# Performance work log

Hardware: AMD Instinct MI355X
Metric: run time of the kernel (lower is better)

The kernel has to match this reference:

```python
import jax, jax.numpy as jnp
import numpy as np

L, H, D, DK, FF = 3, 8, 128, 16, 512  # layers, heads, embed, key/val dim, ffn hidden
B, N, F_IN, OUT = 32, 512, 16, 3
SCALE = 1.0 / np.sqrt(DK)


def setup_inputs() -> dict:
    key = jax.random.key(0)
    ks = jax.random.split(key, 16)
    x = jax.random.normal(ks[0], (B, N, F_IN), dtype=jnp.float32)
    m = jax.random.randint(ks[1], (B, N, N), 0, 2).astype(jnp.int32)
    # guarantee each query attends to at least itself (avoid all -inf rows)
    m = jnp.maximum(m, jnp.eye(N, dtype=jnp.int32)[None])
    def u(k, shape, fan):
        s = 1.0 / np.sqrt(fan)
        return jax.random.uniform(k, shape, jnp.float32, -s, s)
    return {
        "x": x, "mask": m,
        "We": u(ks[2], (F_IN, D), D),
        "Wq": u(ks[3], (L, H, D, DK), DK),
        "Wk": u(ks[4], (L, H, D, DK), DK),
        "Wv": u(ks[5], (L, H, D, DK), DK),
        "Wout": u(ks[6], (L, H, DK, D), D),
        "Wff1": u(ks[7], (L, D, FF), D),
        "bff1": u(ks[8], (L, FF), D),
        "Wff2": u(ks[9], (L, FF, D), FF),
        "bff2": u(ks[10], (L, D), FF),
        "Wp": u(ks[11], (D, D), D),
        "Wr": u(ks[12], (2 * D, OUT), 2 * D),
        "br": u(ks[13], (OUT,), 2 * D),
    }


def reference(x, mask, We, Wq, Wk, Wv, Wout, Wff1, bff1, Wff2, bff2, Wp, Wr, br):
    mb = mask.astype(bool)[None]  # [1,B,N,N] broadcast over heads
    h = jax.nn.relu(x @ We)  # initial embedding [B,N,D]
    for l in range(L):
        # multi-head attention with additive skip
        Q = jnp.einsum('bnd,hdk->hbnk', h, Wq[l])
        K = jnp.einsum('bnd,hdk->hbnk', h, Wk[l])
        V = jnp.einsum('bnd,hdk->hbnk', h, Wv[l])
        compat = SCALE * jnp.einsum('hbqk,hbnk->hbqn', Q, K)  # [H,B,N,N]
        compat = jnp.where(mb, compat, -jnp.inf)
        attn = jax.nn.softmax(compat, axis=-1)
        # note: torch's attn.clone()[...] = 0 is a no-op, so no re-zeroing
        heads = jnp.einsum('hbqn,hbnk->hbqk', attn, V)
        h = h + jnp.einsum('hbqk,hkd->bqd', heads, Wout[l])
        # feed-forward with additive skip
        h = h + jax.nn.relu(h @ Wff1[l] + bff1[l]) @ Wff2[l] + bff2[l] * 0 + (jax.nn.relu(h @ Wff1[l] + bff1[l]) @ Wff2[l] + bff2[l] - (jax.nn.relu(h @ Wff1[l] + bff1[l]) @ Wff2[l]))  # placeholder removed below
    return h


# clean faithful version (used)
def reference(x, mask, We, Wq, Wk, Wv, Wout, Wff1, bff1, Wff2, bff2, Wp, Wr, br):
    mb = mask.astype(bool)[None]  # [1,B,N,N]
    h = jax.nn.relu(x @ We)  # [B,N,D]
    for l in range(L):
        Q = jnp.einsum('bnd,hdk->hbnk', h, Wq[l])
        K = jnp.einsum('bnd,hdk->hbnk', h, Wk[l])
        V = jnp.einsum('bnd,hdk->hbnk', h, Wv[l])
        compat = SCALE * jnp.einsum('hbqk,hbnk->hbqn', Q, K)
        compat = jnp.where(mb, compat, -jnp.inf)
        attn = jax.nn.softmax(compat, axis=-1)
        heads = jnp.einsum('hbqn,hbnk->hbqk', attn, V)
        h = h + jnp.einsum('hbqk,hkd->bqd', heads, Wout[l])
        h = h + (jax.nn.relu(h @ Wff1[l] + bff1[l]) @ Wff2[l] + bff2[l])
    # readout (actor head: output_dim=3)
    h_pooled = (h.mean(axis=1)) @ Wp  # [B,D]
    f_pooled = jnp.broadcast_to(h_pooled[:, None, :], h.shape)  # [B,N,D]
    features = jax.nn.relu(jnp.concatenate([f_pooled, h], axis=-1))  # [B,N,2D]
    return features @ Wr + br  # [B,N,3]
```

## Files before the change

### kernel.cpp

```cpp
#include <hip/hip_runtime.h>
#include <cstdint>
#include <cstddef>

#define L_LAYERS 3
#define H_HEADS 8
#define D_EMB 128
#define DKV 16
#define FF_DIM 512
#define B_BATCH 32
#define N_SEQ 512
#define F_INP 16
#define OUT_DIM 3
#define M_ROWS (B_BATCH * N_SEQ)
#define QSCALE 0.3606737602222409f

typedef unsigned short ushort_t;
typedef unsigned int uint_t;
typedef __attribute__((ext_vector_type(8))) short short8;
typedef __attribute__((ext_vector_type(4))) float f32x4;
typedef __attribute__((ext_vector_type(16))) float f32x16;

__device__ inline ushort_t f2bf(float x) {
    union { float f; uint_t u; } v; v.f = x;
    uint_t r = v.u + 0x7fffu + ((v.u >> 16) & 1u);
    return (ushort_t)(r >> 16);
}

__device__ inline uint_t pack2bf_tr(float a, float b) {
    union { float f; uint_t u; } ua, ub;
    ua.f = a; ub.f = b;
    return (ua.u >> 16) | (ub.u & 0xffff0000u);
}

__device__ inline float exp2fast(float x) {
#if __has_builtin(__builtin_amdgcn_exp2f)
    return __builtin_amdgcn_exp2f(x);
#else
    float r; __asm__("v_exp_f32 %0, %1" : "=v"(r) : "v"(x)); return r;
#endif
}

__device__ inline void gload16(const void* g, void* l) {
    __builtin_amdgcn_global_load_lds(
        (const __attribute__((address_space(1))) unsigned int*)g,
        (__attribute__((address_space(3))) unsigned int*)l, 16, 0, 0);
}

#define PM_BLK 32768
#define RQ_BLK 576
#define TW_BLK 192
#define T1_BLK 768
#define T2_BLK 768
#define PB_BLK 16
#define EM_BLK 8192
__global__ __launch_bounds__(256) void preproc_kernel(
        const int* __restrict__ mask, unsigned long long* __restrict__ pm,
        const float* __restrict__ Wq, const float* __restrict__ Wk,
        const float* __restrict__ Wv, ushort_t* __restrict__ wqkvT,
        const float* __restrict__ Wout, ushort_t* __restrict__ woutT,
        const float* __restrict__ Wff1, ushort_t* __restrict__ wff1T,
        const float* __restrict__ Wff2, ushort_t* __restrict__ wff2T,
        float* __restrict__ pbsum,
        const float* __restrict__ x, const float* __restrict__ We,
        float* __restrict__ hf, ushort_t* __restrict__ hb) {
    int bx = blockIdx.x;
    const int tid = threadIdx.x;
    if (bx < PM_BLK) {
        int gid = bx * 256 + tid;
        int v = mask[gid];
        unsigned long long bal = __ballot(v != 0);
        if ((tid & 63) == 0) pm[gid >> 6] = bal;
        return;
    }
    bx -= PM_BLK;
    if (bx < RQ_BLK) {
        int idx = bx * 256 + tid;
        int d = idx & 127;
        int n = (idx >> 7) % 384;
        int l = idx / (384 * 128);
        int proj = n >> 7, hh = (n & 127) >> 4, kk = n & 15;
        const float* src = proj == 0 ? Wq : proj == 1 ? Wk : Wv;
        wqkvT[idx] = f2bf(src[((size_t)(l * 8 + hh) * 128 + d) * 16 + kk]);
        return;
    }
    bx -= RQ_BLK;
    if (bx < TW_BLK + T1_BLK + T2_BLK) {
        const float* src; ushort_t* dst; int R, C;
        if (bx < TW_BLK) { src = Wout; dst = woutT; R = 128; C = 128; }
        else if (bx < TW_BLK + T1_BLK) { src = Wff1; dst = wff1T; R = 128; C = 512; bx -= TW_BLK; }
        else { src = Wff2; dst = wff2T; R = 512; C = 128; bx -= TW_BLK + T1_BLK; }
        int idx = bx * 256 + tid;
        int b = idx / (R * C);
        int rem = idx - b * (R * C);
        int r = rem / C, c = rem - r * C;
        dst[(size_t)b * R * C + (size_t)c * R + r] = f2bf(src[idx]);
        return;
    }
    bx -= TW_BLK + T1_BLK + T2_BLK;
    if (bx < PB_BLK) {
        pbsum[bx * 256 + tid] = 0.f;
        return;
    }
    bx -= PB_BLK;
    {
        const int d = tid & 127;
        const int m = bx * 2 + (tid >> 7);
        const float* xr = x + (size_t)m * 16;
        float acc = 0.f;
#pragma unroll
        for (int k = 0; k < 16; k++) acc += xr[k] * We[k * 128 + d];
        acc = fmaxf(acc, 0.f);
        hf[(size_t)m * 128 + d] = acc;
        hb[(size_t)m * 128 + d] = f2bf(acc);
    }
}

__global__ __launch_bounds__(512, 2) void qkv_attn_kernel(
        const ushort_t* __restrict__ hb,
        const ushort_t* __restrict__ WqkvT,
        const uint_t* __restrict__ pm,
        ushort_t* __restrict__ Aout) {
    __shared__ __align__(16) ushort_t sm[26752];
    ushort_t* KF = sm;
    ushort_t* Vt = sm + 8192;
    ushort_t* Qs = sm + 16512;
    ushort_t* Ws = sm + 20608;
    ushort_t* Ps = sm + 16512;

    const int tid = threadIdx.x;
    const int w = tid >> 6, L = tid & 63;
    const int lr = L & 15, lq = L >> 4;
    const int lane31 = L & 31, lhalf = L >> 5;
    const int bx = blockIdx.x;
    const int b = bx >> 4, h = (bx >> 1) & 7, half = bx & 1;

    for (int i = tid; i < 768; i += 512) {
        const int row = i >> 4, cg = i & 15;
        const int proj = row >> 4, kk = row & 15;
        gload16(WqkvT + (size_t)(proj * 128 + h * 16 + kk) * 128 + cg * 8, &Ws[i * 8]);
    }
    __syncthreads();

    const ushort_t* Ab = hb + (size_t)b * 512 * 128;
    for (int mc = 0; mc < 4; mc++) {
        f32x4 acc[3];
#pragma unroll
        for (int j = 0; j < 3; j++) acc[j] = (f32x4){0.f, 0.f, 0.f, 0.f};
#pragma unroll
        for (int k0 = 0; k0 < 128; k0 += 32) {
            short8 af = *(const short8*)(Ab + (size_t)(mc * 128 + w * 16 + lr) * 128 + k0 + lq * 8);
#pragma unroll
            for (int j = 0; j < 3; j++) {
                short8 bf = *(const short8*)&Ws[(j * 16 + lr) * 128 + k0 + lq * 8];
                acc[j] = __builtin_amdgcn_mfma_f32_16x16x32_bf16(af, bf, acc[j], 0, 0, 0);
            }
        }
        const int rbase = mc * 128 + w * 16 + lq * 4;
#pragma unroll
        for (int r = 0; r < 4; r++) {
            const int key = rbase + r;
            KF[(key >> 5) * 512 + ((lr >> 3) * 32 + (key & 31)) * 8 + (lr & 7)] = f2bf(acc[1][r]);
            Vt[lr * 520 + key] = f2bf(acc[2][r]);
        }
        if ((mc >> 1) == half) {
            const int qb = (mc & 1) * 128 + w * 16 + lq * 4;
#pragma unroll
            for (int r = 0; r < 4; r++)
                Qs[(qb + r) * 16 + lr] = f2bf(acc[0][r] * QSCALE);
        }
    }
    __syncthreads();

    const int q0g = half * 256 + w * 32;
    const short8 qf = *(const short8*)&Qs[(w * 32 + lane31) * 16 + lhalf * 8];
    const uint_t* pmr = pm + (size_t)(b * 512 + q0g + lane31) * 16;
    const uint4 mwa = *(const uint4*)(pmr);
    const uint4 mwb = *(const uint4*)(pmr + 4);
    const uint4 mwc = *(const uint4*)(pmr + 8);
    const uint4 mwd = *(const uint4*)(pmr + 12);
    const uint_t mw[16] = {mwa.x, mwa.y, mwa.z, mwa.w, mwb.x, mwb.y, mwb.z, mwb.w,
                           mwc.x, mwc.y, mwc.z, mwc.w, mwd.x, mwd.y, mwd.z, mwd.w};
    __syncthreads();

    const f32x16 zero16 = (f32x16)(0.f);
    short8 vone;
#pragma unroll
    for (int i = 0; i < 8; i++) vone[i] = (short)0x3F80;

    f32x4 oacc0 = (f32x4){0.f, 0.f, 0.f, 0.f};
    f32x4 oacc1 = (f32x4){0.f, 0.f, 0.f, 0.f};
    f32x4 lacc0 = (f32x4){0.f, 0.f, 0.f, 0.f};
    f32x4 lacc1 = (f32x4){0.f, 0.f, 0.f, 0.f};
#pragma unroll
    for (int t = 0; t < 16; t++) {
        short8 kf = *(const short8*)&KF[t * 512 + L * 8];
        f32x16 s = __builtin_amdgcn_mfma_f32_32x32x16_bf16(kf, qf, zero16, 0, 0, 0);
        const uint_t word = mw[t];
#pragma unroll
        for (int r = 0; r < 16; r++) {
            const int keyl = (r & 3) + 8 * (r >> 2) + 4 * lhalf;
            const float e = exp2fast(s[r]);
            s[r] = (word & (1u << keyl)) ? e : 0.f;
        }
#pragma unroll
        for (int g = 0; g < 4; g++) {
            const uint_t lo = pack2bf_tr(s[g * 4 + 0], s[g * 4 + 1]);
            const uint_t hi = pack2bf_tr(s[g * 4 + 2], s[g * 4 + 3]);
            *(uint2*)&Ps[w * 1152 + lane31 * 36 + g * 8 + 4 * lhalf] = make_uint2(lo, hi);
        }
        short8 vb = *(const short8*)&Vt[lr * 520 + t * 32 + lq * 8];
        short8 pa0 = *(const short8*)&Ps[w * 1152 + lr * 36 + lq * 8];
        short8 pa1 = *(const short8*)&Ps[w * 1152 + (16 + lr) * 36 + lq * 8];
        oacc0 = __builtin_amdgcn_mfma_f32_16x16x32_bf16(pa0, vb, oacc0, 0, 0, 0);
        oacc1 = __builtin_amdgcn_mfma_f32_16x16x32_bf16(pa1, vb, oacc1, 0, 0, 0);
        lacc0 = __builtin_amdgcn_mfma_f32_16x16x32_bf16(pa0, vone, lacc0, 0, 0, 0);
        lacc1 = __builtin_amdgcn_mfma_f32_16x16x32_bf16(pa1, vone, lacc1, 0, 0, 0);
    }

#pragma unroll
    for (int qa = 0; qa < 2; qa++) {
        const f32x4 oa = qa ? oacc1 : oacc0;
        const f32x4 la = qa ? lacc1 : lacc0;
#pragma unroll
        for (int rr = 0; rr < 4; rr++) {
            const int qloc = qa * 16 + lq * 4 + rr;
            Aout[(size_t)(b * 512 + q0g + qloc) * 128 + h * 16 + lr] = f2bf(oa[rr] / la[rr]);
        }
    }
}

__global__ __launch_bounds__(256, 2) void tail_kernel(
        const ushort_t* __restrict__ A,
        const ushort_t* __restrict__ WoT,
        const ushort_t* __restrict__ W1T,
        const ushort_t* __restrict__ W2T,
        const float* __restrict__ b1,
        const float* __restrict__ b2,
        float* __restrict__ hf, ushort_t* __restrict__ hb,
        float* __restrict__ pbsum, int accum) {
    __shared__ __align__(16) ushort_t sm[38400];
    ushort_t* As  = sm;
    ushort_t* Bs  = sm + 1024;
    ushort_t* C1b = sm + 17408;
    ushort_t* T   = sm + 21760;

    const int tid = threadIdx.x;
    const int w = tid >> 6, l = tid & 63;
    const int lr = l & 15, lq = l >> 4;
    const int srow = (l >> 2);
    const int scol = (l & 3) * 8;
    const int m0 = blockIdx.x * 32;

    f32x4 c1a[2][2];
#pragma unroll
    for (int i = 0; i < 2; i++)
#pragma unroll
        for (int j = 0; j < 2; j++) c1a[i][j] = (f32x4){0.f, 0.f, 0.f, 0.f};
    for (int k0 = 0; k0 < 128; k0 += 32) {
        if (w < 2)
            gload16(A + (size_t)(m0 + w * 16 + srow) * 128 + k0 + scol,
                    &As[(w * 16 + srow) * 32 + scol]);
#pragma unroll
        for (int it = 0; it < 2; it++)
            gload16(WoT + (size_t)(it * 64 + w * 16 + srow) * 128 + k0 + scol,
                    &Bs[(it * 64 + w * 16 + srow) * 32 + scol]);
        __syncthreads();
        short8 af[2], bfr[2];
#pragma unroll
        for (int i = 0; i < 2; i++) af[i] = *(const short8*)&As[(i * 16 + lr) * 32 + lq * 8];
#pragma unroll
        for (int j = 0; j < 2; j++) bfr[j] = *(const short8*)&Bs[(w * 32 + j * 16 + lr) * 32 + lq * 8];
#pragma unroll
        for (int i = 0; i < 2; i++)
#pragma unroll
            for (int j = 0; j < 2; j++)
                c1a[i][j] = __builtin_amdgcn_mfma_f32_16x16x32_bf16(af[i], bfr[j], c1a[i][j], 0, 0, 0);
        __syncthreads();
    }
    float c1[2][2][4];
#pragma unroll
    for (int i = 0; i < 2; i++)
#pragma unroll
        for (int r = 0; r < 4; r++) {
            const int row = i * 16 + lq * 4 + r;
#pragma unroll
            for (int j = 0; j < 2; j++) {
                const int n = w * 32 + j * 16 + lr;
                const float v = c1a[i][j][r] + hf[(size_t)(m0 + row) * 128 + n];
                c1[i][j][r] = v;
                C1b[row * 136 + n] = f2bf(v);
            }
        }
    __syncthreads();

    f32x4 ta[2][8];
#pragma unroll
    for (int i = 0; i < 2; i++)
#pragma unroll
        for (int j = 0; j < 8; j++) ta[i][j] = (f32x4){0.f, 0.f, 0.f, 0.f};
    for (int k0 = 0; k0 < 128; k0 += 32) {
#pragma unroll
        for (int it = 0; it < 8; it++)
            gload16(W1T + (size_t)(it * 64 + w * 16 + srow) * 128 + k0 + scol,
                    &Bs[(it * 64 + w * 16 + srow) * 32 + scol]);
        __syncthreads();
        short8 af[2], bfr[8];
#pragma unroll
        for (int i = 0; i < 2; i++) af[i] = *(const short8*)&C1b[(i * 16 + lr) * 136 + k0 + lq * 8];
#pragma unroll
        for (int j = 0; j < 8; j++) bfr[j] = *(const short8*)&Bs[(w * 128 + j * 16 + lr) * 32 + lq * 8];
#pragma unroll
        for (int i = 0; i < 2; i++)
#pragma unroll
            for (int j = 0; j < 8; j++)
                ta[i][j] = __builtin_amdgcn_mfma_f32_16x16x32_bf16(af[i], bfr[j], ta[i][j], 0, 0, 0);
        __syncthreads();
    }
#pragma unroll
    for (int j = 0; j < 8; j++) {
        const int n = w * 128 + j * 16 + lr;
        const float bv = b1[n];
#pragma unroll
        for (int i = 0; i < 2; i++)
#pragma unroll
            for (int r = 0; r < 4; r++) {
                const int row = i * 16 + lq * 4 + r;
                T[row * 520 + n] = f2bf(fmaxf(ta[i][j][r] + bv, 0.f));
            }
    }
    __syncthreads();

    f32x4 oa[2][2];
#pragma unroll
    for (int i = 0; i < 2; i++)
#pragma unroll
        for (int j = 0; j < 2; j++) oa[i][j] = (f32x4){0.f, 0.f, 0.f, 0.f};
    for (int k0 = 0; k0 < 512; k0 += 32) {
#pragma unroll
        for (int it = 0; it < 2; it++)
            gload16(W2T + (size_t)(it * 64 + w * 16 + srow) * 512 + k0 + scol,
                    &Bs[(it * 64 + w * 16 + srow) * 32 + scol]);
        __syncthreads();
        short8 af[2], bfr[2];
#pragma unroll
        for (int i = 0; i < 2; i++) af[i] = *(const short8*)&T[(i * 16 + lr) * 520 + k0 + lq * 8];
#pragma unroll
        for (int j = 0; j < 2; j++) bfr[j] = *(const short8*)&Bs[(w * 32 + j * 16 + lr) * 32 + lq * 8];
#pragma unroll
        for (int i = 0; i < 2; i++)
#pragma unroll
            for (int j = 0; j < 2; j++)
                oa[i][j] = __builtin_amdgcn_mfma_f32_16x16x32_bf16(af[i], bfr[j], oa[i][j], 0, 0, 0);
        __syncthreads();
    }
#pragma unroll
    for (int j = 0; j < 2; j++) {
        const int n = w * 32 + j * 16 + lr;
        const float bv = b2[n];
        float psum = 0.f;
#pragma unroll
        for (int i = 0; i < 2; i++)
#pragma unroll
            for (int r = 0; r < 4; r++) {
                const int row = i * 16 + lq * 4 + r;
                const float v = oa[i][j][r] + bv + c1[i][j][r];
                psum += v;
                hf[(size_t)(m0 + row) * 128 + n] = v;
                hb[(size_t)(m0 + row) * 128 + n] = f2bf(v);
            }
        if (accum) {
            psum += __shfl_xor(psum, 16);
            psum += __shfl_xor(psum, 32);
            if (lq == 0) atomicAdd(&pbsum[(m0 >> 9) * 128 + n], psum);
        }
    }
}

__global__ __launch_bounds__(256) void readout_kernel(const float* __restrict__ h,
                                                      const float* __restrict__ pbsum,
                                                      const float* __restrict__ Wp,
                                                      const float* __restrict__ Wr,
                                                      const float* __restrict__ br,
                                                      float* __restrict__ out) {
    const int u = blockIdx.x;
    const int b = u >> 4;
    const int m0 = u * 32;
    const int t = threadIdx.x;
    __shared__ float pooled[128];
    __shared__ float rp[128];
    __shared__ float pb3[3];
    if (t < 128) pooled[t] = pbsum[b * 128 + t] * (1.0f / 512.0f);
    __syncthreads();
    if (t < 128) {
        float a = 0.f;
        for (int dd = 0; dd < 128; dd++) a += pooled[dd] * Wp[dd * 128 + t];
        rp[t] = fmaxf(a, 0.f);
    }
    __syncthreads();
    if (t < OUT_DIM) {
        float a = br[t];
        for (int j = 0; j < 128; j++) a += rp[j] * Wr[j * 3 + t];
        pb3[t] = a;
    }
    __syncthreads();
    const int j = t & 7;
    const int row = m0 + (t >> 3);
    const float* hr = h + (size_t)row * 128 + j * 16;
    float a0 = 0.f, a1 = 0.f, a2o = 0.f;
#pragma unroll
    for (int dd = 0; dd < 16; dd++) {
        const float v = fmaxf(hr[dd], 0.f);
        const float* wr = Wr + (size_t)(128 + j * 16 + dd) * 3;
        a0 += v * wr[0]; a1 += v * wr[1]; a2o += v * wr[2];
    }
#pragma unroll
    for (int off = 4; off; off >>= 1) {
        a0 += __shfl_down(a0, off, 8);
        a1 += __shfl_down(a1, off, 8);
        a2o += __shfl_down(a2o, off, 8);
    }
    if (j == 0) {
        out[(size_t)row * 3 + 0] = a0 + pb3[0];
        out[(size_t)row * 3 + 1] = a1 + pb3[1];
        out[(size_t)row * 3 + 2] = a2o + pb3[2];
    }
}

extern "C" void kernel_launch(void* const* d_in, const int* in_sizes, int n_in,
                              void* d_out, int out_size, void* d_ws, size_t ws_size,
                              hipStream_t stream) {
    const float* x    = (const float*)d_in[0];
    const int*   mask = (const int*)d_in[1];
    const float* We   = (const float*)d_in[2];
    const float* Wq   = (const float*)d_in[3];
    const float* Wk   = (const float*)d_in[4];
    const float* Wv   = (const float*)d_in[5];
    const float* Wout = (const float*)d_in[6];
    const float* Wff1 = (const float*)d_in[7];
    const float* bff1 = (const float*)d_in[8];
    const float* Wff2 = (const float*)d_in[9];
    const float* bff2 = (const float*)d_in[10];
    const float* Wp   = (const float*)d_in[11];
    const float* Wr   = (const float*)d_in[12];
    const float* br   = (const float*)d_in[13];
    float* out = (float*)d_out;

    char* ws = (char*)d_ws;
    unsigned long long* pm64 = (unsigned long long*)(ws + 0);
    const uint_t* pm32       = (const uint_t*)(ws + 0);
    ushort_t* wqkvT = (ushort_t*)(ws + 1048576);
    ushort_t* woutT = (ushort_t*)(ws + 1343488);
    ushort_t* wff1T = (ushort_t*)(ws + 1441792);
    ushort_t* wff2T = (ushort_t*)(ws + 1835008);
    float*    pbsum = (float*)(ws + 2228224);
    float*    hbuf  = (float*)(ws + 4194304);
    ushort_t* hb16  = (ushort_t*)(ws + 12582912);
    ushort_t* a16   = (ushort_t*)(ws + 41943040);

    preproc_kernel<<<PM_BLK + RQ_BLK + TW_BLK + T1_BLK + T2_BLK + PB_BLK + EM_BLK, 256, 0, stream>>>(
        mask, pm64, Wq, Wk, Wv, wqkvT, Wout, woutT, Wff1, wff1T, Wff2, wff2T,
        pbsum, x, We, hbuf, hb16);

    for (int l = 0; l < L_LAYERS; l++) {
        qkv_attn_kernel<<<512, 512, 0, stream>>>(
            hb16, wqkvT + (size_t)l * 384 * 128, pm32, a16);
        tail_kernel<<<M_ROWS / 32, 256, 0, stream>>>(
            a16, woutT + (size_t)l * 128 * 128, wff1T + (size_t)l * 512 * 128,
            wff2T + (size_t)l * 128 * 512, bff1 + l * 512, bff2 + l * 128,
            hbuf, hb16, pbsum, (l == L_LAYERS - 1) ? 1 : 0);
    }

    readout_kernel<<<512, 256, 0, stream>>>(hbuf, pbsum, Wp, Wr, br, out);
}
```

Before: 277.0 us.

## Double-buffer weight tiles in tail kernel and split FF1 into two column halves

Converts the three GEMM stages in tail_kernel to double-buffered shared-memory staging. Each iteration prefetches the next K-slice of A/WoT, W1T or W2T into the alternate buffer, which overlaps global loads with MFMA work and leaves one barrier per iteration instead of two. To fit two W1T buffers, the FF1 stage is split into two 256-column halves with half as many accumulators. Shared memory grows slightly, and the prefetch issued right before the C1b and T writes relies on the next loop's barrier for ordering.

```diff
diff --git a/kernel.cpp b/kernel.cpp
--- a/kernel.cpp
+++ b/kernel.cpp
@@ -238,11 +238,13 @@
         const float* __restrict__ b2,
         float* __restrict__ hf, ushort_t* __restrict__ hb,
         float* __restrict__ pbsum, int accum) {
-    __shared__ __align__(16) ushort_t sm[38400];
-    ushort_t* As  = sm;
-    ushort_t* Bs  = sm + 1024;
-    ushort_t* C1b = sm + 17408;
-    ushort_t* T   = sm + 21760;
+    __shared__ __align__(16) ushort_t sm[39424];
+    ushort_t* AsA = sm;
+    ushort_t* AsB = sm + 1024;
+    ushort_t* BsA = sm + 2048;
+    ushort_t* BsB = sm + 10240;
+    ushort_t* C1b = sm + 18432;
+    ushort_t* T   = sm + 22784;
 
     const int tid = threadIdx.x;
     const int w = tid >> 6, l = tid & 63;
@@ -256,26 +258,37 @@
     for (int i = 0; i < 2; i++)
 #pragma unroll
         for (int j = 0; j < 2; j++) c1a[i][j] = (f32x4){0.f, 0.f, 0.f, 0.f};
+    if (w < 2)
+        gload16(A + (size_t)(m0 + w * 16 + srow) * 128 + scol, &AsA[(w * 16 + srow) * 32 + scol]);
+#pragma unroll
+    for (int it = 0; it < 2; it++)
+        gload16(WoT + (size_t)(it * 64 + w * 16 + srow) * 128 + scol, &BsA[(it * 64 + w * 16 + srow) * 32 + scol]);
+#pragma unroll
     for (int k0 = 0; k0 < 128; k0 += 32) {
-        if (w < 2)
-            gload16(A + (size_t)(m0 + w * 16 + srow) * 128 + k0 + scol,
-                    &As[(w * 16 + srow) * 32 + scol]);
-#pragma unroll
-        for (int it = 0; it < 2; it++)
-            gload16(WoT + (size_t)(it * 64 + w * 16 + srow) * 128 + k0 + scol,
-                    &Bs[(it * 64 + w * 16 + srow) * 32 + scol]);
+        ushort_t* Ac = (k0 & 32) ? AsB : AsA;
+        ushort_t* Bc = (k0 & 32) ? BsB : BsA;
+        ushort_t* An = (k0 & 32) ? AsA : AsB;
+        ushort_t* Bn = (k0 & 32) ? BsA : BsB;
         __syncthreads();
+        if (k0 + 32 < 128) {
+            if (w < 2)
+                gload16(A + (size_t)(m0 + w * 16 + srow) * 128 + k0 + 32 + scol,
+                        &An[(w * 16 + srow) * 32 + scol]);
+#pragma unroll
+            for (int it = 0; it < 2; it++)
+                gload16(WoT + (size_t)(it * 64 + w * 16 + srow) * 128 + k0 + 32 + scol,
+                        &Bn[(it * 64 + w * 16 + srow) * 32 + scol]);
+        }
         short8 af[2], bfr[2];
 #pragma unroll
-        for (int i = 0; i < 2; i++) af[i] = *(const short8*)&As[(i * 16 + lr) * 32 + lq * 8];
-#pragma unroll
-        for (int j = 0; j < 2; j++) bfr[j] = *(const short8*)&Bs[(w * 32 + j * 16 + lr) * 32 + lq * 8];
+        for (int i = 0; i < 2; i++) af[i] = *(const short8*)&Ac[(i * 16 + lr) * 32 + lq * 8];
+#pragma unroll
+        for (int j = 0; j < 2; j++) bfr[j] = *(const short8*)&Bc[(w * 32 + j * 16 + lr) * 32 + lq * 8];
 #pragma unroll
         for (int i = 0; i < 2; i++)
 #pragma unroll
             for (int j = 0; j < 2; j++)
                 c1a[i][j] = __builtin_amdgcn_mfma_f32_16x16x32_bf16(af[i], bfr[j], c1a[i][j], 0, 0, 0);
-        __syncthreads();
     }
     float c1[2][2][4];
 #pragma unroll
@@ -291,67 +304,88 @@
                 C1b[row * 136 + n] = f2bf(v);
             }
         }
-    __syncthreads();
-
-    f32x4 ta[2][8];
+
+#pragma unroll
+    for (int it = 0; it < 4; it++)
+        gload16(W1T + (size_t)(it * 64 + w * 16 + srow) * 128 + scol, &BsA[(it * 64 + w * 16 + srow) * 32 + scol]);
+#pragma unroll
+    for (int nc = 0; nc < 2; nc++) {
+        f32x4 ta[2][4];
+#pragma unroll
+        for (int i = 0; i < 2; i++)
+#pragma unroll
+            for (int j = 0; j < 4; j++) ta[i][j] = (f32x4){0.f, 0.f, 0.f, 0.f};
+#pragma unroll
+        for (int k0i = 0; k0i < 4; k0i++) {
+            const int c = nc * 4 + k0i;
+            ushort_t* Bc = (c & 1) ? BsB : BsA;
+            ushort_t* Bn = (c & 1) ? BsA : BsB;
+            __syncthreads();
+            if (c + 1 < 8) {
+                const int nc2 = (c + 1) >> 2, k02 = ((c + 1) & 3) * 32;
+#pragma unroll
+                for (int it = 0; it < 4; it++)
+                    gload16(W1T + (size_t)(nc2 * 256 + it * 64 + w * 16 + srow) * 128 + k02 + scol,
+                            &Bn[(it * 64 + w * 16 + srow) * 32 + scol]);
+            }
+            short8 af[2], bfr[4];
+#pragma unroll
+            for (int i = 0; i < 2; i++)
+                af[i] = *(const short8*)&C1b[(i * 16 + lr) * 136 + k0i * 32 + lq * 8];
+#pragma unroll
+            for (int j = 0; j < 4; j++)
+                bfr[j] = *(const short8*)&Bc[(w * 64 + j * 16 + lr) * 32 + lq * 8];
+#pragma unroll
+            for (int i = 0; i < 2; i++)
+#pragma unroll
+                for (int j = 0; j < 4; j++)
+                    ta[i][j] = __builtin_amdgcn_mfma_f32_16x16x32_bf16(af[i], bfr[j], ta[i][j], 0, 0, 0);
+        }
+#pragma unroll
+        for (int j = 0; j < 4; j++) {
+            const int n = nc * 256 + w * 64 + j * 16 + lr;
+            const float bv = b1[n];
+#pragma unroll
+            for (int i = 0; i < 2; i++)
+#pragma unroll
+                for (int r = 0; r < 4; r++) {
+                    const int row = i * 16 + lq * 4 + r;
+                    T[row * 520 + n] = f2bf(fmaxf(ta[i][j][r] + bv, 0.f));
+                }
+        }
+    }
+
+#pragma unroll
+    for (int it = 0; it < 2; it++)
+        gload16(W2T + (size_t)(it * 64 + w * 16 + srow) * 512 + scol, &BsA[(it * 64 + w * 16 + srow) * 32 + scol]);
+    f32x4 oa[2][2];
 #pragma unroll
     for (int i = 0; i < 2; i++)
 #pragma unroll
-        for (int j = 0; j < 8; j++) ta[i][j] = (f32x4){0.f, 0.f, 0.f, 0.f};
-    for (int k0 = 0; k0 < 128; k0 += 32) {
-#pragma unroll
-        for (int it = 0; it < 8; it++)
-            gload16(W1T + (size_t)(it * 64 + w * 16 + srow) * 128 + k0 + scol,
-                    &Bs[(it * 64 + w * 16 + srow) * 32 + scol]);
+        for (int j = 0; j < 2; j++) oa[i][j] = (f32x4){0.f, 0.f, 0.f, 0.f};
+#pragma unroll
+    for (int k0 = 0; k0 < 512; k0 += 32) {
+        ushort_t* Bc = ((k0 >> 5) & 1) ? BsB : BsA;
+        ushort_t* Bn = ((k0 >> 5) & 1) ? BsA : BsB;
         __syncthreads();
-        short8 af[2], bfr[8];
-#pragma unroll
-        for (int i = 0; i < 2; i++) af[i] = *(const short8*)&C1b[(i * 16 + lr) * 136 + k0 + lq * 8];
-#pragma unroll
-        for (int j = 0; j < 8; j++) bfr[j] = *(const short8*)&Bs[(w * 128 + j * 16 + lr) * 32 + lq * 8];
+        if (k0 + 32 < 512) {
+#pragma unroll
+            for (int it = 0; it < 2; it++)
+                gload16(W2T + (size_t)(it * 64 + w * 16 + srow) * 512 + k0 + 32 + scol,
+                        &Bn[(it * 64 + w * 16 + srow) * 32 + scol]);
+        }
+        short8 af[2], bfr[2];
 #pragma unroll
         for (int i = 0; i < 2; i++)
-#pragma unroll
-            for (int j = 0; j < 8; j++)
-                ta[i][j] = __builtin_amdgcn_mfma_f32_16x16x32_bf16(af[i], bfr[j], ta[i][j], 0, 0, 0);
-        __syncthreads();
-    }
-#pragma unroll
-    for (int j = 0; j < 8; j++) {
-        const int n = w * 128 + j * 16 + lr;
-        const float bv = b1[n];
-#pragma unroll
-        for (int i = 0; i < 2; i++)
-#pragma unroll
-            for (int r = 0; r < 4; r++) {
-                const int row = i * 16 + lq * 4 + r;
-                T[row * 520 + n] = f2bf(fmaxf(ta[i][j][r] + bv, 0.f));
-            }
-    }
-    __syncthreads();
-
-    f32x4 oa[2][2];
-#pragma unroll
-    for (int i = 0; i < 2; i++)
-#pragma unroll
-        for (int j = 0; j < 2; j++) oa[i][j] = (f32x4){0.f, 0.f, 0.f, 0.f};
-    for (int k0 = 0; k0 < 512; k0 += 32) {
-#pragma unroll
-        for (int it = 0; it < 2; it++)
-            gload16(W2T + (size_t)(it * 64 + w * 16 + srow) * 512 + k0 + scol,
-                    &Bs[(it * 64 + w * 16 + srow) * 32 + scol]);
-        __syncthreads();
-        short8 af[2], bfr[2];
-#pragma unroll
-        for (int i = 0; i < 2; i++) af[i] = *(const short8*)&T[(i * 16 + lr) * 520 + k0 + lq * 8];
-#pragma unroll
-        for (int j = 0; j < 2; j++) bfr[j] = *(const short8*)&Bs[(w * 32 + j * 16 + lr) * 32 + lq * 8];
+            af[i] = *(const short8*)&T[(i * 16 + lr) * 520 + k0 + lq * 8];
+#pragma unroll
+        for (int j = 0; j < 2; j++)
+            bfr[j] = *(const short8*)&Bc[(w * 32 + j * 16 + lr) * 32 + lq * 8];
 #pragma unroll
         for (int i = 0; i < 2; i++)
 #pragma unroll
             for (int j = 0; j < 2; j++)
                 oa[i][j] = __builtin_amdgcn_mfma_f32_16x16x32_bf16(af[i], bfr[j], oa[i][j], 0, 0, 0);
-        __syncthreads();
     }
 #pragma unroll
     for (int j = 0; j < 2; j++) {
```

New measurement: 268.7 us. 1.03x faster.
